# Kernel optimization log

Hardware: AMD Instinct MI355X
Metric: run time of the kernel (lower is better)

The kernel has to match this reference:

```python
import jax, jax.numpy as jnp
import numpy as np

HEADS = 16
LN_EPS = 1e-5

def _ln(v, w, b):
    # LayerNorm over last dim (head dim s)
    mu = jnp.mean(v, axis=-1, keepdims=True)
    var = jnp.mean(jnp.square(v - mu), axis=-1, keepdims=True)
    return (v - mu) * jax.lax.rsqrt(var + LN_EPS) * w + b

def setup_inputs() -> dict:
    key = jax.random.key(0)
    ks = jax.random.split(key, 5)
    b, t, e = 2, 2048, 1024
    x = jax.random.normal(ks[0], (b, t, e), dtype=jnp.float32)
    scale = 0.02
    Wk = jax.random.normal(ks[1], (e, e), dtype=jnp.float32) * scale
    Wq = jax.random.normal(ks[2], (e, e), dtype=jnp.float32) * scale
    Wv = jax.random.normal(ks[3], (e, e), dtype=jnp.float32) * scale
    Wu = jax.random.normal(ks[4], (e, e), dtype=jnp.float32) * scale
    s = e // HEADS
    return {
        "x": x, "Wk": Wk, "Wq": Wq, "Wv": Wv, "Wu": Wu,
        "kln_w": jnp.ones((s,), jnp.float32), "kln_b": jnp.zeros((s,), jnp.float32),
        "qln_w": jnp.ones((s,), jnp.float32), "qln_b": jnp.zeros((s,), jnp.float32),
    }

def reference(x, Wk, Wq, Wv, Wu, kln_w, kln_b, qln_w, qln_b):
    b, t, e = x.shape
    h = HEADS
    s = e // h
    # nn.Linear: y = x @ W^T
    k = (x @ Wk.T).reshape(b, t, h, s)
    q = (x @ Wq.T).reshape(b, t, h, s)
    v = (x @ Wv.T).reshape(b, t, h, s)
    k = _ln(k, kln_w, kln_b)
    q = _ln(q, qln_w, qln_b)
    scalefactor = 1.0 / np.sqrt(s).astype(np.float32)
    # [b, h, t_q, t_k]
    dot = jnp.einsum('bqhs,bkhs->bhqk', q, k) * scalefactor
    causal = jnp.triu(jnp.ones((t, t), dtype=bool), k=1)  # mask strictly-upper (diag kept)
    dot = jnp.where(causal, -jnp.inf, dot)
    attn = jax.nn.softmax(dot, axis=-1)
    out = jnp.einsum('bhqk,bkhs->bqhs', attn, v).reshape(b, t, e)
    return out @ Wu.T
```

## Files before the change

kernel.cpp:

```cpp
#include <hip/hip_runtime.h>
#include <math.h>

#define T_SEQ 2048
#define E_DIM 1024
#define NH    16
#define HS    64
#define NB    2
#define M_ROWS 4096

typedef __attribute__((ext_vector_type(8))) short bf16x8;
typedef __attribute__((ext_vector_type(4))) short bf16x4;
typedef __attribute__((ext_vector_type(4))) float f32x4;

#define AS1 __attribute__((address_space(1)))
#define AS3 __attribute__((address_space(3)))

#define LOG2E 1.4426950408889634f

__device__ __forceinline__ f32x4 mfma16(bf16x4 a, bf16x4 b, f32x4 c) {
    return __builtin_amdgcn_mfma_f32_16x16x16bf16_1k(a, b, c, 0, 0, 0);
}

__device__ __forceinline__ ushort f2bf(float f) {
    union { float f; unsigned u; } c; c.f = f;
    unsigned r = c.u + 0x7fffu + ((c.u >> 16) & 1u);
    return (ushort)(r >> 16);
}
__device__ __forceinline__ ushort f2bf_trunc(float f) {
    union { float f; unsigned u; } c; c.f = f;
    return (ushort)(c.u >> 16);
}

__device__ __forceinline__ void load_lds16(const ushort* g, ushort* l) {
    __builtin_amdgcn_global_load_lds((const AS1 unsigned int*)g,
                                     (AS3 unsigned int*)l, 16, 0, 0);
}

__global__ __launch_bounds__(256) void cvt_all(
    const float* __restrict__ x,  const float* __restrict__ Wk,
    const float* __restrict__ Wq, const float* __restrict__ Wv,
    const float* __restrict__ Wu,
    ushort* __restrict__ xb,  ushort* __restrict__ Wkb,
    ushort* __restrict__ Wqb, ushort* __restrict__ Wvb,
    ushort* __restrict__ Wub)
{
    int i4 = blockIdx.x * 256 + threadIdx.x;
    int region = i4 >> 18;
    const float* src; ushort* dst; int off;
    if      (region < 4)  { src = x;  dst = xb;  off = i4; }
    else if (region == 4) { src = Wk; dst = Wkb; off = i4 - (4 << 18); }
    else if (region == 5) { src = Wq; dst = Wqb; off = i4 - (5 << 18); }
    else if (region == 6) { src = Wv; dst = Wvb; off = i4 - (6 << 18); }
    else                  { src = Wu; dst = Wub; off = i4 - (7 << 18); }
    float4 v = *(const float4*)(src + (size_t)off * 4);
    ushort4 o; o.x = f2bf(v.x); o.y = f2bf(v.y); o.z = f2bf(v.z); o.w = f2bf(v.w);
    *(ushort4*)(dst + (size_t)off * 4) = o;
}

__device__ __forceinline__ void gemm_core_db(
    const ushort* __restrict__ A, const ushort* __restrict__ W,
    int m0, int n0, ushort* As, ushort* Bs, f32x4 acc[4][4])
{
    const int tid  = threadIdx.x;
    const int lane = tid & 63, w = tid >> 6;
    const int quad = lane >> 4, l16 = lane & 15;
    const int wm = w & 1, wn = w >> 1;

    const int rl   = lane >> 2;
    const int gsw  = (lane & 3) ^ ((lane >> 3) & 3);
    const int fsw  = (l16 >> 1) & 3;

    const f32x4 zero = {0.f, 0.f, 0.f, 0.f};
#pragma unroll
    for (int mt = 0; mt < 4; ++mt)
#pragma unroll
        for (int nt = 0; nt < 4; ++nt) acc[mt][nt] = zero;

#pragma unroll
    for (int i = 0; i < 2; ++i) {
        int c = i * 4 + w;
        int row = c * 16 + rl;
        load_lds16(A + (size_t)(m0 + row) * E_DIM + gsw * 8, As + c * 512);
        load_lds16(W + (size_t)(n0 + row) * E_DIM + gsw * 8, Bs + c * 512);
    }

    for (int k0 = 0; k0 < E_DIM; k0 += 32) {
        const int buf = (k0 >> 5) & 1;
        ushort* Ab = As + buf * 4096;
        ushort* Bb = Bs + buf * 4096;
        __syncthreads();
        if (k0 + 32 < E_DIM) {
            ushort* An = As + (buf ^ 1) * 4096;
            ushort* Bn = Bs + (buf ^ 1) * 4096;
#pragma unroll
            for (int i = 0; i < 2; ++i) {
                int c = i * 4 + w;
                int row = c * 16 + rl;
                load_lds16(A + (size_t)(m0 + row) * E_DIM + k0 + 32 + gsw * 8,
                           An + c * 512);
                load_lds16(W + (size_t)(n0 + row) * E_DIM + k0 + 32 + gsw * 8,
                           Bn + c * 512);
            }
        }
        bf16x8 af[4], bfr[4];
#pragma unroll
        for (int mt = 0; mt < 4; ++mt)
            af[mt] = *(const bf16x8*)(Ab + (wm * 64 + mt * 16 + l16) * 32
                                      + ((quad ^ fsw) * 8));
#pragma unroll
        for (int nt = 0; nt < 4; ++nt)
            bfr[nt] = *(const bf16x8*)(Bb + (wn * 64 + nt * 16 + l16) * 32
                                       + ((quad ^ fsw) * 8));
#pragma unroll
        for (int mt = 0; mt < 4; ++mt)
#pragma unroll
            for (int nt = 0; nt < 4; ++nt)
                acc[mt][nt] = __builtin_amdgcn_mfma_f32_16x16x32_bf16(
                    af[mt], bfr[nt], acc[mt][nt], 0, 0, 0);
    }
}

__global__ __launch_bounds__(256) void gemm_qkv(
    const ushort* __restrict__ A,
    const ushort* __restrict__ W0, const ushort* __restrict__ W1,
    const ushort* __restrict__ W2,
    ushort* __restrict__ Kb, ushort* __restrict__ Qb, ushort* __restrict__ Vt,
    const float* __restrict__ kw, const float* __restrict__ kbias,
    const float* __restrict__ qw, const float* __restrict__ qbias)
{
    __shared__ ushort As[2 * 128 * 32];
    __shared__ ushort Bs[2 * 128 * 32];
    const int z = blockIdx.z;
    const ushort* W = (z == 0) ? W0 : (z == 1) ? W1 : W2;
    const int m0 = blockIdx.y * 128, n0 = blockIdx.x * 128;
    f32x4 acc[4][4];
    gemm_core_db(A, W, m0, n0, As, Bs, acc);

    const int lane = threadIdx.x & 63, w = threadIdx.x >> 6;
    const int quad = lane >> 4, l16 = lane & 15;
    const int wm = w & 1, wn = w >> 1;
    const int row0 = m0 + wm * 64;
    const int col0 = n0 + wn * 64;

    if (z < 2) {
        ushort* C = z ? Qb : Kb;
        const float* lw = z ? qw : kw;
        const float* lb = z ? qbias : kbias;
        const float scale = z ? (0.125f * LOG2E) : 1.0f;
        float wv[4], bv_[4];
#pragma unroll
        for (int nt = 0; nt < 4; ++nt) {
            wv[nt]  = lw[nt * 16 + l16];
            bv_[nt] = lb[nt * 16 + l16];
        }
#pragma unroll
        for (int mt = 0; mt < 4; ++mt)
#pragma unroll
            for (int r = 0; r < 4; ++r) {
                float v[4], d[4];
#pragma unroll
                for (int nt = 0; nt < 4; ++nt) v[nt] = acc[mt][nt][r];
                float s = v[0] + v[1] + v[2] + v[3];
                s += __shfl_xor(s, 1); s += __shfl_xor(s, 2);
                s += __shfl_xor(s, 4); s += __shfl_xor(s, 8);
                float mu = s * (1.0f / 64.0f);
                float q2 = 0.f;
#pragma unroll
                for (int nt = 0; nt < 4; ++nt) { d[nt] = v[nt] - mu; q2 += d[nt] * d[nt]; }
                q2 += __shfl_xor(q2, 1); q2 += __shfl_xor(q2, 2);
                q2 += __shfl_xor(q2, 4); q2 += __shfl_xor(q2, 8);
                float rin = rsqrtf(q2 * (1.0f / 64.0f) + 1e-5f);
                int row = row0 + mt * 16 + quad * 4 + r;
#pragma unroll
                for (int nt = 0; nt < 4; ++nt)
                    C[(size_t)row * E_DIM + col0 + nt * 16 + l16] =
                        f2bf((d[nt] * rin * wv[nt] + bv_[nt]) * scale);
            }
    } else {
        const int bidx = m0 >> 11;
        const int hh   = col0 >> 6;
        const int t0   = (m0 & 2047) + wm * 64;
#pragma unroll
        for (int mt = 0; mt < 4; ++mt)
#pragma unroll
            for (int nt = 0; nt < 4; ++nt) {
                ushort4 pk = make_ushort4(f2bf(acc[mt][nt][0]), f2bf(acc[mt][nt][1]),
                                          f2bf(acc[mt][nt][2]), f2bf(acc[mt][nt][3]));
                size_t off = ((size_t)(bidx * NH + hh) * 64 + nt * 16 + l16) * T_SEQ
                             + t0 + mt * 16 + quad * 4;
                *(ushort4*)(Vt + off) = pk;
            }
    }
}

__global__ __launch_bounds__(256) void gemm_o(
    const ushort* __restrict__ A, const ushort* __restrict__ W,
    float* __restrict__ C)
{
    __shared__ ushort As[2 * 128 * 32];
    __shared__ ushort Bs[2 * 128 * 32];
    const int m0 = blockIdx.y * 128, n0 = blockIdx.x * 128;
    f32x4 acc[4][4];
    gemm_core_db(A, W, m0, n0, As, Bs, acc);

    const int lane = threadIdx.x & 63, w = threadIdx.x >> 6;
    const int quad = lane >> 4, l16 = lane & 15;
    const int row0 = m0 + (w & 1) * 64;
    const int col0 = n0 + (w >> 1) * 64;
#pragma unroll
    for (int mt = 0; mt < 4; ++mt)
#pragma unroll
        for (int nt = 0; nt < 4; ++nt)
#pragma unroll
            for (int r = 0; r < 4; ++r)
                C[(size_t)(row0 + mt * 16 + quad * 4 + r) * E_DIM
                  + col0 + nt * 16 + l16] = acc[mt][nt][r];
}

__global__ __launch_bounds__(256, 4) void flash_attn5(
    const ushort* __restrict__ Qg, const ushort* __restrict__ Kg,
    const ushort* __restrict__ Vt, ushort* __restrict__ O)
{
    __shared__ ushort Ks[2][64 * 64];
    __shared__ ushort Vs[2][64 * 64];

    const int tid  = threadIdx.x;
    const int lane = tid & 63, w = tid >> 6;
    const int quad = lane >> 4, l16 = lane & 15;

    const int L = blockIdx.x;
    const int c = L & 255, s = L >> 8;
    const int q0 = c >> 5;
    const int bh = c & 31;
    const int qt = (s == 0) ? q0 : (s == 1) ? (15 - q0)
                 : (s == 2) ? (16 + q0) : (31 - q0);
    const int b = bh >> 4, h = bh & 15;

    const ushort* Qbase = Qg + ((size_t)b * T_SEQ) * E_DIM + h * HS;
    const ushort* Kbase = Kg + ((size_t)b * T_SEQ) * E_DIM + h * HS;
    const ushort* Vbase = Vt + ((size_t)bh * HS) * T_SEQ;

    const int rloc = lane >> 3;
    const int gswc = (lane & 7) ^ rloc;
    const int sw   = l16 & 7;

    bf16x8 aq[2];
#pragma unroll
    for (int ks = 0; ks < 2; ++ks)
        aq[ks] = *(const bf16x8*)(Qbase + (size_t)(qt * 64 + w * 16 + l16) * E_DIM
                                  + ks * 32 + quad * 8);

    const f32x4 zero = {0.f, 0.f, 0.f, 0.f};
    f32x4 o_acc[4];
#pragma unroll
    for (int dt = 0; dt < 4; ++dt) o_acc[dt] = zero;
    float l_acc = 0.f;

#pragma unroll
    for (int i = 0; i < 2; ++i) {
        int cc = w * 2 + i, row = cc * 8 + rloc;
        load_lds16(Kbase + (size_t)row * E_DIM + gswc * 8, Ks[0] + cc * 512);
        load_lds16(Vbase + (size_t)row * T_SEQ + gswc * 8, Vs[0] + cc * 512);
    }

    const float M8 = 8.0f * LOG2E;

    for (int jt = 0; jt <= qt; ++jt) {
        const int buf = jt & 1;
        __syncthreads();
        if (jt < qt) {
#pragma unroll
            for (int i = 0; i < 2; ++i) {
                int cc = w * 2 + i, row = cc * 8 + rloc;
                load_lds16(Kbase + (size_t)(jt + 1) * 64 * E_DIM
                           + (size_t)row * E_DIM + gswc * 8, Ks[buf ^ 1] + cc * 512);
                load_lds16(Vbase + (size_t)row * T_SEQ + (jt + 1) * 64 + gswc * 8,
                           Vs[buf ^ 1] + cc * 512);
            }
        }

        f32x4 sa[4];
#pragma unroll
        for (int nt = 0; nt < 4; ++nt) sa[nt] = zero;
#pragma unroll
        for (int ks = 0; ks < 2; ++ks) {
            int cp = ((ks * 4 + quad) ^ sw) * 8;
#pragma unroll
            for (int nt = 0; nt < 4; ++nt) {
                bf16x8 bk = *(const bf16x8*)(Ks[buf] + (nt * 16 + l16) * 64 + cp);
                sa[nt] = __builtin_amdgcn_mfma_f32_16x16x32_bf16(bk, aq[ks], sa[nt], 0, 0, 0);
            }
        }

        if (jt == qt) {
#pragma unroll
            for (int nt = 0; nt < 4; ++nt)
#pragma unroll
                for (int r = 0; r < 4; ++r)
                    if (nt * 16 + quad * 4 + r > w * 16 + l16) sa[nt][r] = -1e30f;
        }

        bf16x4 bp[4];
#pragma unroll
        for (int nt = 0; nt < 4; ++nt)
#pragma unroll
            for (int r = 0; r < 4; ++r) {
                float p = __builtin_amdgcn_exp2f(sa[nt][r] - M8);
                l_acc += p;
                bp[nt][r] = (short)f2bf_trunc(p);
            }

#pragma unroll
        for (int kt = 0; kt < 4; ++kt) {
            const int tt = kt * 16 + quad * 4;
            const int ch = tt >> 3, el = tt & 7;
#pragma unroll
            for (int dt = 0; dt < 4; ++dt) {
                const int vd = dt * 16 + l16;
                bf16x4 va = *(const bf16x4*)(Vs[buf] + vd * 64
                                             + ((ch ^ (vd & 7)) << 3) + el);
                o_acc[dt] = mfma16(va, bp[kt], o_acc[dt]);
            }
        }
    }

    l_acc += __shfl_xor(l_acc, 16);
    l_acc += __shfl_xor(l_acc, 32);
    const float inv = 1.0f / l_acc;
    const int trow = qt * 64 + w * 16 + l16;
#pragma unroll
    for (int dt = 0; dt < 4; ++dt) {
        ushort4 pk = make_ushort4(f2bf(o_acc[dt][0] * inv), f2bf(o_acc[dt][1] * inv),
                                  f2bf(o_acc[dt][2] * inv), f2bf(o_acc[dt][3] * inv));
        *(ushort4*)(O + ((size_t)b * T_SEQ + trow) * E_DIM + h * HS
                    + dt * 16 + quad * 4) = pk;
    }
}

extern "C" void kernel_launch(void* const* d_in, const int* in_sizes, int n_in,
                              void* d_out, int out_size, void* d_ws, size_t ws_size,
                              hipStream_t stream) {
    const float* x     = (const float*)d_in[0];
    const float* Wk    = (const float*)d_in[1];
    const float* Wq    = (const float*)d_in[2];
    const float* Wv    = (const float*)d_in[3];
    const float* Wu    = (const float*)d_in[4];
    const float* kln_w = (const float*)d_in[5];
    const float* kln_b = (const float*)d_in[6];
    const float* qln_w = (const float*)d_in[7];
    const float* qln_b = (const float*)d_in[8];
    float* out = (float*)d_out;

    const size_t NE = (size_t)M_ROWS * E_DIM;
    const size_t NW = (size_t)E_DIM * E_DIM;
    ushort* xb  = (ushort*)d_ws;
    ushort* Wkb = xb  + NE;
    ushort* Wqb = Wkb + NW;
    ushort* Wvb = Wqb + NW;
    ushort* Wub = Wvb + NW;
    ushort* Kb  = Wub + NW;
    ushort* Qb  = Kb  + NE;
    ushort* Vt  = Qb  + NE;
    ushort* Ob  = Vt  + NE;

    cvt_all<<<8192, 256, 0, stream>>>(x, Wk, Wq, Wv, Wu, xb, Wkb, Wqb, Wvb, Wub);

    gemm_qkv<<<dim3(E_DIM / 128, M_ROWS / 128, 3), 256, 0, stream>>>(
        xb, Wkb, Wqb, Wvb, Kb, Qb, Vt, kln_w, kln_b, qln_w, qln_b);

    flash_attn5<<<1024, 256, 0, stream>>>(Qb, Kb, Vt, Ob);

    gemm_o<<<dim3(E_DIM / 128, M_ROWS / 128), 256, 0, stream>>>(Ob, Wub, out);
}
```

Baseline: 181.5 us.

## Fuse K/Q/V projections into one GEMM block sharing the A tile

Replaces the three separate QKV GEMM blocks (grid z=3) with a single kernel where each block computes K, Q and V for the same 128x128 output tile. The shared x tile is loaded once and reused across three weight tiles, which cuts A-tile global and LDS traffic. The cost is 192 accumulator floats per thread, more LDS (32 KB per block), launch_bounds(256,1) and a grid of only 256 blocks, which lowers occupancy and may spill. The flash attention row-sum is also split into four independent partial accumulators to shorten the dependency chain.

```diff
diff --git a/kernel.cpp b/kernel.cpp
--- a/kernel.cpp
+++ b/kernel.cpp
@@ -57,20 +57,157 @@
     *(ushort4*)(dst + (size_t)off * 4) = o;
 }
 
-__device__ __forceinline__ void gemm_core_db(
-    const ushort* __restrict__ A, const ushort* __restrict__ W,
-    int m0, int n0, ushort* As, ushort* Bs, f32x4 acc[4][4])
+__global__ __launch_bounds__(256, 1) void gemm_qkv3(
+    const ushort* __restrict__ A,
+    const ushort* __restrict__ W0, const ushort* __restrict__ W1,
+    const ushort* __restrict__ W2,
+    ushort* __restrict__ Kb, ushort* __restrict__ Qb, ushort* __restrict__ Vt,
+    const float* __restrict__ kw, const float* __restrict__ kbias,
+    const float* __restrict__ qw, const float* __restrict__ qbias)
 {
+    __shared__ ushort As[2][128 * 32];
+    __shared__ ushort Bs[3][2][128 * 32];
+
     const int tid  = threadIdx.x;
     const int lane = tid & 63, w = tid >> 6;
     const int quad = lane >> 4, l16 = lane & 15;
     const int wm = w & 1, wn = w >> 1;
+    const int m0 = blockIdx.y * 128, n0 = blockIdx.x * 128;
 
     const int rl   = lane >> 2;
     const int gsw  = (lane & 3) ^ ((lane >> 3) & 3);
     const int fsw  = (l16 >> 1) & 3;
 
     const f32x4 zero = {0.f, 0.f, 0.f, 0.f};
+    f32x4 acc[3][4][4];
+#pragma unroll
+    for (int z = 0; z < 3; ++z)
+#pragma unroll
+        for (int mt = 0; mt < 4; ++mt)
+#pragma unroll
+            for (int nt = 0; nt < 4; ++nt) acc[z][mt][nt] = zero;
+
+#pragma unroll
+    for (int i = 0; i < 2; ++i) {
+        int ch = i * 4 + w, row = ch * 16 + rl;
+        load_lds16(A  + (size_t)(m0 + row) * E_DIM + gsw * 8, As[0]    + ch * 512);
+        load_lds16(W0 + (size_t)(n0 + row) * E_DIM + gsw * 8, Bs[0][0] + ch * 512);
+        load_lds16(W1 + (size_t)(n0 + row) * E_DIM + gsw * 8, Bs[1][0] + ch * 512);
+        load_lds16(W2 + (size_t)(n0 + row) * E_DIM + gsw * 8, Bs[2][0] + ch * 512);
+    }
+
+    for (int k0 = 0; k0 < E_DIM; k0 += 32) {
+        const int buf = (k0 >> 5) & 1;
+        __syncthreads();
+        if (k0 + 32 < E_DIM) {
+#pragma unroll
+            for (int i = 0; i < 2; ++i) {
+                int ch = i * 4 + w, row = ch * 16 + rl;
+                load_lds16(A  + (size_t)(m0 + row) * E_DIM + k0 + 32 + gsw * 8,
+                           As[buf ^ 1]    + ch * 512);
+                load_lds16(W0 + (size_t)(n0 + row) * E_DIM + k0 + 32 + gsw * 8,
+                           Bs[0][buf ^ 1] + ch * 512);
+                load_lds16(W1 + (size_t)(n0 + row) * E_DIM + k0 + 32 + gsw * 8,
+                           Bs[1][buf ^ 1] + ch * 512);
+                load_lds16(W2 + (size_t)(n0 + row) * E_DIM + k0 + 32 + gsw * 8,
+                           Bs[2][buf ^ 1] + ch * 512);
+            }
+        }
+        bf16x8 af[4];
+#pragma unroll
+        for (int mt = 0; mt < 4; ++mt)
+            af[mt] = *(const bf16x8*)(As[buf] + (wm * 64 + mt * 16 + l16) * 32
+                                      + ((quad ^ fsw) * 8));
+#pragma unroll
+        for (int z = 0; z < 3; ++z) {
+            bf16x8 bfr[4];
+#pragma unroll
+            for (int nt = 0; nt < 4; ++nt)
+                bfr[nt] = *(const bf16x8*)(Bs[z][buf]
+                          + (wn * 64 + nt * 16 + l16) * 32 + ((quad ^ fsw) * 8));
+#pragma unroll
+            for (int mt = 0; mt < 4; ++mt)
+#pragma unroll
+                for (int nt = 0; nt < 4; ++nt)
+                    acc[z][mt][nt] = __builtin_amdgcn_mfma_f32_16x16x32_bf16(
+                        af[mt], bfr[nt], acc[z][mt][nt], 0, 0, 0);
+        }
+    }
+
+    const int row0 = m0 + wm * 64;
+    const int col0 = n0 + wn * 64;
+
+#pragma unroll
+    for (int z = 0; z < 2; ++z) {
+        ushort* C = z ? Qb : Kb;
+        const float* lw = z ? qw : kw;
+        const float* lb = z ? qbias : kbias;
+        const float scale = z ? (0.125f * LOG2E) : 1.0f;
+        float wv[4], bv_[4];
+#pragma unroll
+        for (int nt = 0; nt < 4; ++nt) {
+            wv[nt]  = lw[nt * 16 + l16];
+            bv_[nt] = lb[nt * 16 + l16];
+        }
+#pragma unroll
+        for (int mt = 0; mt < 4; ++mt)
+#pragma unroll
+            for (int r = 0; r < 4; ++r) {
+                float v[4], d[4];
+#pragma unroll
+                for (int nt = 0; nt < 4; ++nt) v[nt] = acc[z][mt][nt][r];
+                float s = v[0] + v[1] + v[2] + v[3];
+                s += __shfl_xor(s, 1); s += __shfl_xor(s, 2);
+                s += __shfl_xor(s, 4); s += __shfl_xor(s, 8);
+                float mu = s * (1.0f / 64.0f);
+                float q2 = 0.f;
+#pragma unroll
+                for (int nt = 0; nt < 4; ++nt) { d[nt] = v[nt] - mu; q2 += d[nt] * d[nt]; }
+                q2 += __shfl_xor(q2, 1); q2 += __shfl_xor(q2, 2);
+                q2 += __shfl_xor(q2, 4); q2 += __shfl_xor(q2, 8);
+                float rin = rsqrtf(q2 * (1.0f / 64.0f) + 1e-5f);
+                int row = row0 + mt * 16 + quad * 4 + r;
+#pragma unroll
+                for (int nt = 0; nt < 4; ++nt)
+                    C[(size_t)row * E_DIM + col0 + nt * 16 + l16] =
+                        f2bf((d[nt] * rin * wv[nt] + bv_[nt]) * scale);
+            }
+    }
+    {
+        const int bidx = m0 >> 11;
+        const int hh   = col0 >> 6;
+        const int t0   = (m0 & 2047) + wm * 64;
+#pragma unroll
+        for (int mt = 0; mt < 4; ++mt)
+#pragma unroll
+            for (int nt = 0; nt < 4; ++nt) {
+                ushort4 pk = make_ushort4(f2bf(acc[2][mt][nt][0]), f2bf(acc[2][mt][nt][1]),
+                                          f2bf(acc[2][mt][nt][2]), f2bf(acc[2][mt][nt][3]));
+                size_t off = ((size_t)(bidx * NH + hh) * 64 + nt * 16 + l16) * T_SEQ
+                             + t0 + mt * 16 + quad * 4;
+                *(ushort4*)(Vt + off) = pk;
+            }
+    }
+}
+
+__global__ __launch_bounds__(256) void gemm_o(
+    const ushort* __restrict__ A, const ushort* __restrict__ W,
+    float* __restrict__ C)
+{
+    __shared__ ushort As[2 * 128 * 32];
+    __shared__ ushort Bs[2 * 128 * 32];
+    const int tid  = threadIdx.x;
+    const int lane = tid & 63, w = tid >> 6;
+    const int quad = lane >> 4, l16 = lane & 15;
+    const int wm = w & 1, wn = w >> 1;
+    const int m0 = blockIdx.y * 128, n0 = blockIdx.x * 128;
+
+    const int rl   = lane >> 2;
+    const int gsw  = (lane & 3) ^ ((lane >> 3) & 3);
+    const int fsw  = (l16 >> 1) & 3;
+
+    const f32x4 zero = {0.f, 0.f, 0.f, 0.f};
+    f32x4 acc[4][4];
 #pragma unroll
     for (int mt = 0; mt < 4; ++mt)
 #pragma unroll
@@ -78,8 +215,7 @@
 
 #pragma unroll
     for (int i = 0; i < 2; ++i) {
-        int c = i * 4 + w;
-        int row = c * 16 + rl;
+        int c = i * 4 + w, row = c * 16 + rl;
         load_lds16(A + (size_t)(m0 + row) * E_DIM + gsw * 8, As + c * 512);
         load_lds16(W + (size_t)(n0 + row) * E_DIM + gsw * 8, Bs + c * 512);
     }
@@ -94,8 +230,7 @@
             ushort* Bn = Bs + (buf ^ 1) * 4096;
 #pragma unroll
             for (int i = 0; i < 2; ++i) {
-                int c = i * 4 + w;
-                int row = c * 16 + rl;
+                int c = i * 4 + w, row = c * 16 + rl;
                 load_lds16(A + (size_t)(m0 + row) * E_DIM + k0 + 32 + gsw * 8,
                            An + c * 512);
                 load_lds16(W + (size_t)(n0 + row) * E_DIM + k0 + 32 + gsw * 8,
@@ -118,95 +253,9 @@
                 acc[mt][nt] = __builtin_amdgcn_mfma_f32_16x16x32_bf16(
                     af[mt], bfr[nt], acc[mt][nt], 0, 0, 0);
     }
-}
-
-__global__ __launch_bounds__(256) void gemm_qkv(
-    const ushort* __restrict__ A,
-    const ushort* __restrict__ W0, const ushort* __restrict__ W1,
-    const ushort* __restrict__ W2,
-    ushort* __restrict__ Kb, ushort* __restrict__ Qb, ushort* __restrict__ Vt,
-    const float* __restrict__ kw, const float* __restrict__ kbias,
-    const float* __restrict__ qw, const float* __restrict__ qbias)
-{
-    __shared__ ushort As[2 * 128 * 32];
-    __shared__ ushort Bs[2 * 128 * 32];
-    const int z = blockIdx.z;
-    const ushort* W = (z == 0) ? W0 : (z == 1) ? W1 : W2;
-    const int m0 = blockIdx.y * 128, n0 = blockIdx.x * 128;
-    f32x4 acc[4][4];
-    gemm_core_db(A, W, m0, n0, As, Bs, acc);
-
-    const int lane = threadIdx.x & 63, w = threadIdx.x >> 6;
-    const int quad = lane >> 4, l16 = lane & 15;
-    const int wm = w & 1, wn = w >> 1;
+
     const int row0 = m0 + wm * 64;
     const int col0 = n0 + wn * 64;
-
-    if (z < 2) {
-        ushort* C = z ? Qb : Kb;
-        const float* lw = z ? qw : kw;
-        const float* lb = z ? qbias : kbias;
-        const float scale = z ? (0.125f * LOG2E) : 1.0f;
-        float wv[4], bv_[4];
-#pragma unroll
-        for (int nt = 0; nt < 4; ++nt) {
-            wv[nt]  = lw[nt * 16 + l16];
-            bv_[nt] = lb[nt * 16 + l16];
-        }
-#pragma unroll
-        for (int mt = 0; mt < 4; ++mt)
-#pragma unroll
-            for (int r = 0; r < 4; ++r) {
-                float v[4], d[4];
-#pragma unroll
-                for (int nt = 0; nt < 4; ++nt) v[nt] = acc[mt][nt][r];
-                float s = v[0] + v[1] + v[2] + v[3];
-                s += __shfl_xor(s, 1); s += __shfl_xor(s, 2);
-                s += __shfl_xor(s, 4); s += __shfl_xor(s, 8);
-                float mu = s * (1.0f / 64.0f);
-                float q2 = 0.f;
-#pragma unroll
-                for (int nt = 0; nt < 4; ++nt) { d[nt] = v[nt] - mu; q2 += d[nt] * d[nt]; }
-                q2 += __shfl_xor(q2, 1); q2 += __shfl_xor(q2, 2);
-                q2 += __shfl_xor(q2, 4); q2 += __shfl_xor(q2, 8);
-                float rin = rsqrtf(q2 * (1.0f / 64.0f) + 1e-5f);
-                int row = row0 + mt * 16 + quad * 4 + r;
-#pragma unroll
-                for (int nt = 0; nt < 4; ++nt)
-                    C[(size_t)row * E_DIM + col0 + nt * 16 + l16] =
-                        f2bf((d[nt] * rin * wv[nt] + bv_[nt]) * scale);
-            }
-    } else {
-        const int bidx = m0 >> 11;
-        const int hh   = col0 >> 6;
-        const int t0   = (m0 & 2047) + wm * 64;
-#pragma unroll
-        for (int mt = 0; mt < 4; ++mt)
-#pragma unroll
-            for (int nt = 0; nt < 4; ++nt) {
-                ushort4 pk = make_ushort4(f2bf(acc[mt][nt][0]), f2bf(acc[mt][nt][1]),
-                                          f2bf(acc[mt][nt][2]), f2bf(acc[mt][nt][3]));
-                size_t off = ((size_t)(bidx * NH + hh) * 64 + nt * 16 + l16) * T_SEQ
-                             + t0 + mt * 16 + quad * 4;
-                *(ushort4*)(Vt + off) = pk;
-            }
-    }
-}
-
-__global__ __launch_bounds__(256) void gemm_o(
-    const ushort* __restrict__ A, const ushort* __restrict__ W,
-    float* __restrict__ C)
-{
-    __shared__ ushort As[2 * 128 * 32];
-    __shared__ ushort Bs[2 * 128 * 32];
-    const int m0 = blockIdx.y * 128, n0 = blockIdx.x * 128;
-    f32x4 acc[4][4];
-    gemm_core_db(A, W, m0, n0, As, Bs, acc);
-
-    const int lane = threadIdx.x & 63, w = threadIdx.x >> 6;
-    const int quad = lane >> 4, l16 = lane & 15;
-    const int row0 = m0 + (w & 1) * 64;
-    const int col0 = n0 + (w >> 1) * 64;
 #pragma unroll
     for (int mt = 0; mt < 4; ++mt)
 #pragma unroll
@@ -254,7 +303,7 @@
     f32x4 o_acc[4];
 #pragma unroll
     for (int dt = 0; dt < 4; ++dt) o_acc[dt] = zero;
-    float l_acc = 0.f;
+    float l4[4] = {0.f, 0.f, 0.f, 0.f};
 
 #pragma unroll
     for (int i = 0; i < 2; ++i) {
@@ -306,7 +355,7 @@
 #pragma unroll
             for (int r = 0; r < 4; ++r) {
                 float p = __builtin_amdgcn_exp2f(sa[nt][r] - M8);
-                l_acc += p;
+                l4[nt] += p;
                 bp[nt][r] = (short)f2bf_trunc(p);
             }
 
@@ -324,6 +373,7 @@
         }
     }
 
+    float l_acc = (l4[0] + l4[1]) + (l4[2] + l4[3]);
     l_acc += __shfl_xor(l_acc, 16);
     l_acc += __shfl_xor(l_acc, 32);
     const float inv = 1.0f / l_acc;
@@ -365,7 +415,7 @@
 
     cvt_all<<<8192, 256, 0, stream>>>(x, Wk, Wq, Wv, Wu, xb, Wkb, Wqb, Wvb, Wub);
 
-    gemm_qkv<<<dim3(E_DIM / 128, M_ROWS / 128, 3), 256, 0, stream>>>(
+    gemm_qkv3<<<dim3(E_DIM / 128, M_ROWS / 128), 256, 0, stream>>>(
         xb, Wkb, Wqb, Wvb, Kb, Qb, Vt, kln_w, kln_b, qln_w, qln_b);
 
     flash_attn5<<<1024, 256, 0, stream>>>(Qb, Kb, Vt, Ob);
```

Measured after the change: 194.9 us. 7.3% more time.
